# Kernel optimization log

Measured on AMD Instinct MI355X. Metric: run time of the kernel, lower is better.

The kernel has to match this reference:

```python
import jax, jax.numpy as jnp
import numpy as np

N_DIRS = 32  # number of projection directions


def gram_schmidt(x):
    # x: [B, n, D]; sequential Gram-Schmidt; normalized basis vectors are
    # detached (stop_gradient) as in the torch original.
    B, n, D = x.shape
    xs = jnp.swapaxes(x, 0, 1)  # [n, B, D]
    basis0 = jnp.zeros((n, B, D), dtype=x.dtype)

    def step(carry, w):
        basis, i = carry

        def proj(j, wv):
            b = basis[j]  # rows >= i are zero and contribute nothing
            return wv - b * jnp.sum(wv * b, axis=-1, keepdims=True)

        w_o = jax.lax.fori_loop(0, n, proj, w)
        w_sg = jax.lax.stop_gradient(w_o)
        w_hat = w_sg / jnp.linalg.norm(w_sg, axis=-1, keepdims=True)
        basis = jax.lax.dynamic_update_slice(basis, w_hat[None], (i, 0, 0))
        return (basis, i + 1), w_o

    (_, _), x_orth = jax.lax.scan(step, (basis0, jnp.int32(0)), xs)
    return jnp.swapaxes(x_orth, 0, 1)  # [B, n, D]


def setup_inputs() -> dict:
    key = jax.random.key(0)
    k = jax.random.split(key, 6)
    B = 2048
    IN_LP = 32 * 26       # 832 = linear_projection_x_dim * 26
    IMG = 28 * 28         # 784
    IN_NET = 2 * IMG      # 1568
    OUT_NET = N_DIRS * IMG  # 25088

    x_distorted = jax.random.normal(k[0], (B, IN_LP), dtype=jnp.float32)
    x_restored = jax.random.uniform(k[1], (B, 1, 28, 28), dtype=jnp.float32)

    s1 = 1.0 / np.sqrt(IN_LP)
    W_lp = jax.random.uniform(k[2], (IMG, IN_LP), jnp.float32, -s1, s1)
    b_lp = jax.random.uniform(k[3], (IMG,), jnp.float32, -s1, s1)

    s2 = 1.0 / np.sqrt(IN_NET)
    W_net = jax.random.uniform(k[4], (OUT_NET, IN_NET), jnp.float32, -s2, s2)
    b_net = jax.random.uniform(k[5], (OUT_NET,), jnp.float32, -s2, s2)

    return {"x_distorted": x_distorted, "x_restored": x_restored,
            "W_lp": W_lp, "b_lp": b_lp, "W_net": W_net, "b_net": b_net}


def reference(x_distorted, x_restored, W_lp, b_lp, W_net, b_net):
    B = x_distorted.shape[0]
    xd = x_distorted.reshape(B, -1) @ W_lp.T + b_lp      # [B, 784]
    xd = xd.reshape(B, 1, 28, 28)
    x = jnp.concatenate([xd, x_restored], axis=1)        # [B, 2, 28, 28]
    x = (x - 0.5) / 0.2
    w_mat = (x.reshape(B, -1) @ W_net.T + b_net) * 0.2   # [B, n_dirs*784]
    w_mat = w_mat.reshape(B, N_DIRS, -1)                 # [B, n_dirs, 784]
    return gram_schmidt(w_mat)
```

## Files before the change

### kernel.cpp

```cpp
#include <hip/hip_runtime.h>
#include <hip/hip_bf16.h>
#include <stdint.h>


typedef short s16x8 __attribute__((ext_vector_type(8)));
typedef float f32x4 __attribute__((ext_vector_type(4)));

#define GL_LDS16(gptr, lptr)                                                   \
    __builtin_amdgcn_global_load_lds(                                          \
        (const __attribute__((address_space(1))) void*)(gptr),                 \
        (__attribute__((address_space(3))) void*)(lptr), 16, 0, 0)

#define KP 1600

__global__ __launch_bounds__(512, 1) void gemm_mfma_256(
    const __hip_bfloat16* __restrict__ A, const __hip_bfloat16* __restrict__ B,
    const float* __restrict__ bias, float* __restrict__ C,
    int M, int N, int K)
{
    __shared__ __align__(16) short lds[2][30720];

    const int t = threadIdx.x;
    const int l = t & 63;
    const int wv = t >> 6;
    const int wm = wv >> 1;
    const int wn = wv & 1;

    const int f  = blockIdx.x;
    const int xb = f >> 3;
    const int yb = f & 7;
    const int m0 = yb * 256;
    const int n0 = xb * 224;

    const short* As = (const short*)A;
    const short* Bs = (const short*)B;

    const bool isA = wv < 4;
    const int colE = (((l & 7) ^ (l >> 3)) << 3);
    const size_t srcRow = isA ? (size_t)(m0 + wv * 64 + (l >> 3))
                              : (size_t)(n0 + (wv - 4) * 56 + (l >> 3));
    const size_t src0 = srcRow * KP + colE;
    const short* gsrc = isA ? As : Bs;
    const int dstBase = isA ? wv * 4096 : 16384 + (wv - 4) * 3584;

    const int sk0 = ((l >> 4) << 3) ^ ((l & 7) << 3);
    const int sk1 = sk0 ^ 32;
    const int aoff = (wm * 64 + (l & 15)) * 64;
    const int boff = 16384 + (wn * 112 + (l & 15)) * 64;

    f32x4 acc[4][7] = {};

#define STAGE_TILE(buf, T)                                                     \
    do {                                                                       \
        short* d_ = &lds[buf][dstBase];                                        \
        const short* s_ = gsrc + src0 + (size_t)(T) * 64;                      \
        GL_LDS16(s_ + (size_t)0 * 8 * KP, d_ + 0 * 512);                       \
        GL_LDS16(s_ + (size_t)1 * 8 * KP, d_ + 1 * 512);                       \
        GL_LDS16(s_ + (size_t)2 * 8 * KP, d_ + 2 * 512);                       \
        GL_LDS16(s_ + (size_t)3 * 8 * KP, d_ + 3 * 512);                       \
        GL_LDS16(s_ + (size_t)4 * 8 * KP, d_ + 4 * 512);                       \
        GL_LDS16(s_ + (size_t)5 * 8 * KP, d_ + 5 * 512);                       \
        GL_LDS16(s_ + (size_t)6 * 8 * KP, d_ + 6 * 512);                       \
        if (isA) GL_LDS16(s_ + (size_t)7 * 8 * KP, d_ + 7 * 512);              \
    } while (0)

    const int NT = K >> 6;
    STAGE_TILE(0, 0);
    __syncthreads();

    for (int kt = 0; kt < NT; ++kt) {
        const int cur = kt & 1;
        const short* bufc = &lds[cur][0];

        if (kt + 1 < NT) STAGE_TILE(cur ^ 1, kt + 1);

        s16x8 bfr[7][2];
        #pragma unroll
        for (int ni = 0; ni < 7; ++ni) {
            bfr[ni][0] = *(const s16x8*)&bufc[boff + ni * 1024 + sk0];
            bfr[ni][1] = *(const s16x8*)&bufc[boff + ni * 1024 + sk1];
        }

        #pragma unroll
        for (int mi = 0; mi < 4; ++mi) {
            s16x8 a0 = *(const s16x8*)&bufc[aoff + mi * 1024 + sk0];
            s16x8 a1 = *(const s16x8*)&bufc[aoff + mi * 1024 + sk1];
            __builtin_amdgcn_s_setprio(1);
            #pragma unroll
            for (int ni = 0; ni < 7; ++ni) {
                acc[mi][ni] = __builtin_amdgcn_mfma_f32_16x16x32_bf16(
                    a0, bfr[ni][0], acc[mi][ni], 0, 0, 0);
                acc[mi][ni] = __builtin_amdgcn_mfma_f32_16x16x32_bf16(
                    a1, bfr[ni][1], acc[mi][ni], 0, 0, 0);
            }
            __builtin_amdgcn_s_setprio(0);
        }

        __syncthreads();
    }
#undef STAGE_TILE

    const int row0 = m0 + wm * 64 + ((l >> 4) << 2);
    const int col0 = n0 + wn * 112 + (l & 15);
    #pragma unroll
    for (int ni = 0; ni < 7; ++ni) {
        const int n = col0 + ni * 16;
        const float bn = bias[n];
        #pragma unroll
        for (int mi = 0; mi < 4; ++mi) {
            const int r0 = row0 + mi * 16;
            #pragma unroll
            for (int r = 0; r < 4; ++r)
                C[(size_t)(r0 + r) * N + n] = (acc[mi][ni][r] + bn) * 0.2f;
        }
    }
}

__global__ __launch_bounds__(256) void wnet_to_bf16(
    const float* __restrict__ in, __hip_bfloat16* __restrict__ out)
{
    const size_t r = blockIdx.x;
    const int t = threadIdx.x;
    const float* src = in + r * 1568;
    __hip_bfloat16* dst = out + r * KP;

    for (int i = t; i < 392; i += 256) {
        float4 v = *(const float4*)(src + (i << 2));
        __hip_bfloat16 o[4] = {
            __float2bfloat16(v.x), __float2bfloat16(v.y),
            __float2bfloat16(v.z), __float2bfloat16(v.w)};
        *(ushort4*)&dst[i << 2] = *(const ushort4*)o;
    }
    if (t < 8)
        *(ushort4*)&dst[1568 + (t << 2)] = make_ushort4(0, 0, 0, 0);
}

#define TILE_M 64
#define TILE_N 64
#define TILE_K 16
#define LDS_STRIDE 72

__global__ __launch_bounds__(256) void gemm_nt_lp(
    const float* __restrict__ A, const float* __restrict__ B,
    const float* __restrict__ bias, __hip_bfloat16* __restrict__ C,
    int M, int N, int K, int ldc)
{
    __shared__ float As[TILE_K][LDS_STRIDE];
    __shared__ float Bsh[TILE_K][LDS_STRIDE];

    const int t  = threadIdx.x;
    const int tx = t & 15;
    const int ty = t >> 4;
    const int m0 = blockIdx.y * TILE_M;
    const int n0 = blockIdx.x * TILE_N;
    const int lrow = t >> 2;
    const int lk   = (t & 3) << 2;

    float acc[4][4] = {};

    for (int kt = 0; kt < K; kt += TILE_K) {
        float4 av = *(const float4*)(A + (size_t)(m0 + lrow) * K + kt + lk);
        float4 bv = make_float4(0.f, 0.f, 0.f, 0.f);
        if (n0 + lrow < N)
            bv = *(const float4*)(B + (size_t)(n0 + lrow) * K + kt + lk);

        __syncthreads();
        As[lk + 0][lrow] = av.x; As[lk + 1][lrow] = av.y;
        As[lk + 2][lrow] = av.z; As[lk + 3][lrow] = av.w;
        Bsh[lk + 0][lrow] = bv.x; Bsh[lk + 1][lrow] = bv.y;
        Bsh[lk + 2][lrow] = bv.z; Bsh[lk + 3][lrow] = bv.w;
        __syncthreads();

        #pragma unroll
        for (int k = 0; k < TILE_K; ++k) {
            float4 a = *(const float4*)&As[k][ty << 2];
            float4 b = *(const float4*)&Bsh[k][tx << 2];
            acc[0][0] += a.x * b.x; acc[0][1] += a.x * b.y;
            acc[0][2] += a.x * b.z; acc[0][3] += a.x * b.w;
            acc[1][0] += a.y * b.x; acc[1][1] += a.y * b.y;
            acc[1][2] += a.y * b.z; acc[1][3] += a.y * b.w;
            acc[2][0] += a.z * b.x; acc[2][1] += a.z * b.y;
            acc[2][2] += a.z * b.z; acc[2][3] += a.z * b.w;
            acc[3][0] += a.w * b.x; acc[3][1] += a.w * b.y;
            acc[3][2] += a.w * b.z; acc[3][3] += a.w * b.w;
        }
    }

    #pragma unroll
    for (int j = 0; j < 4; ++j) {
        int n = n0 + (tx << 2) + j;
        if (n < N) {
            float bn = bias[n];
            #pragma unroll
            for (int i = 0; i < 4; ++i) {
                float v = (acc[i][j] + bn - 0.5f) / 0.2f;
                C[(size_t)(m0 + (ty << 2) + i) * ldc + n] = __float2bfloat16(v);
            }
        }
    }
}

__global__ __launch_bounds__(256) void build_restored(
    const float* __restrict__ xr, __hip_bfloat16* __restrict__ x)
{
    const int b = blockIdx.x;
    const int t = threadIdx.x;
    if (t < 196) {
        float4 v = *(const float4*)(xr + (size_t)b * 784 + (t << 2));
        __hip_bfloat16 o[4] = {
            __float2bfloat16((v.x - 0.5f) / 0.2f),
            __float2bfloat16((v.y - 0.5f) / 0.2f),
            __float2bfloat16((v.z - 0.5f) / 0.2f),
            __float2bfloat16((v.w - 0.5f) / 0.2f)};
        *(ushort4*)&x[(size_t)b * KP + 784 + (t << 2)] = *(const ushort4*)o;
    } else if (t < 204) {
        *(ushort4*)&x[(size_t)b * KP + 1568 + ((t - 196) << 2)] =
            make_ushort4(0, 0, 0, 0);
    }
}

#define GS_N 32
#define GS_D 784

__global__ __launch_bounds__(256, 4) void gram_solve(
    const float* __restrict__ out, float* __restrict__ Mws)
{
    __shared__ __align__(16) short Wc[GS_N * 64];
    __shared__ float Gs[GS_N][GS_N + 1];
    __shared__ float Ms[GS_N][GS_N + 1];
    __shared__ float Ld[GS_N];

    const int t = threadIdx.x;
    const int l = t & 63;
    const int w = t >> 6;
    const float* row0 = out + (size_t)blockIdx.x * (GS_N * GS_D);

    const int wr = w >> 1, wc2 = w & 1;
    const int ra = wr * 16 + (l & 15);
    const int rb = wc2 * 16 + (l & 15);
    const int kg = l >> 4;

    f32x4 acc = {};

    for (int k0 = 0; k0 < 832; k0 += 64) {
        #pragma unroll
        for (int hh = 0; hh < 2; ++hh) {
            const int h   = t + hh * 256;
            const int r   = h >> 4;
            const int hg  = h & 15;
            const int col = k0 + (hg << 2);
            ushort4 u = make_ushort4(0, 0, 0, 0);
            if (col < GS_D) {
                float4 v = *(const float4*)(row0 + r * GS_D + col);
                __hip_bfloat16 hb[4] = {
                    __float2bfloat16(v.x), __float2bfloat16(v.y),
                    __float2bfloat16(v.z), __float2bfloat16(v.w)};
                u = *(const ushort4*)hb;
            }
            const int gp = (hg >> 1) ^ (r & 7);
            *(ushort4*)&Wc[(r << 6) + (gp << 3) + ((hg & 1) << 2)] = u;
        }
        __syncthreads();

        #pragma unroll
        for (int s = 0; s < 2; ++s) {
            const int ga = ((s << 2) + kg) ^ (ra & 7);
            const int gb = ((s << 2) + kg) ^ (rb & 7);
            s16x8 af = *(const s16x8*)&Wc[(ra << 6) + (ga << 3)];
            s16x8 bf = *(const s16x8*)&Wc[(rb << 6) + (gb << 3)];
            acc = __builtin_amdgcn_mfma_f32_16x16x32_bf16(af, bf, acc, 0, 0, 0);
        }
        __syncthreads();
    }

    {
        const int di = wr * 16 + (l >> 4) * 4;
        const int dj = wc2 * 16 + (l & 15);
        #pragma unroll
        for (int r = 0; r < 4; ++r) Gs[di + r][dj] = acc[r];
    }
    for (int z = t; z < GS_N * (GS_N + 1); z += 256) ((float*)Ms)[z] = 0.f;
    __syncthreads();

    for (int k = 0; k < GS_N; ++k) {
        const float sk = sqrtf(Gs[k][k]);
        if (t == k) Ld[k] = sk;
        if (t > k && t < GS_N) Gs[t][k] /= sk;
        __syncthreads();
        if (t > k && t < GS_N) {
            const float lik = Gs[t][k];
            for (int j = k + 1; j <= t; ++j)
                Gs[t][j] -= lik * Gs[j][k];
        }
        __syncthreads();
    }

    if (t < GS_N) {
        const int j = t;
        Ms[j][j] = 1.0f / Ld[j];
        for (int i = j + 1; i < GS_N; ++i) {
            float a = 0.f;
            for (int k = j; k < i; ++k)
                a += Gs[i][k] * Ms[k][j];
            Ms[i][j] = -a / Ld[i];
        }
        for (int i = j + 1; i < GS_N; ++i)
            Ms[i][j] *= Ld[i];
    }
    __syncthreads();

    {
        const int i = t >> 3, j0 = (t & 7) << 2;
        float4 mv = make_float4(Ms[i][j0], Ms[i][j0 + 1],
                                Ms[i][j0 + 2], Ms[i][j0 + 3]);
        *(float4*)(Mws + (size_t)blockIdx.x * 1024 + (t << 2)) = mv;
    }
}

__global__ __launch_bounds__(256, 8) void gs_apply(
    float* __restrict__ out, const float* __restrict__ Mws)
{
    __shared__ float4 Wf[GS_N][28];
    __shared__ float  Ml[GS_N][36];

    const int t = threadIdx.x;
    const int b = blockIdx.y;
    const int k0 = blockIdx.x * 112;
    float* row0 = out + (size_t)b * (GS_N * GS_D);

    {
        float4 mv = *(const float4*)(Mws + (size_t)b * 1024 + (t << 2));
        const int i = t >> 3, j0 = (t & 7) << 2;
        *(float4*)&Ml[i][j0] = mv;
    }
    #pragma unroll
    for (int hh = 0; hh < 4; ++hh) {
        const int h = t + hh * 256;
        const int r = h >> 5, c = h & 31;
        if (c < 28)
            Wf[r][c] = *(const float4*)(row0 + r * GS_D + k0 + (c << 2));
    }
    __syncthreads();

    const int g  = t >> 5;
    const int c4 = t & 31;
    if (c4 < 28) {
        const int rA = g, rB = 31 - g, rC = 15 - g, rD = 16 + g;
        float4 vA = Wf[rA][c4];
        float4 vB = Wf[rB][c4];
        float4 vC = Wf[rC][c4];
        float4 vD = Wf[rD][c4];
        for (int j = 0; j < rB; ++j) {
            const float4 wj = Wf[j][c4];
            const float mA = (j < rA) ? Ml[rA][j] : 0.f;
            const float mB = Ml[rB][j];
            vA.x += mA * wj.x; vA.y += mA * wj.y;
            vA.z += mA * wj.z; vA.w += mA * wj.w;
            vB.x += mB * wj.x; vB.y += mB * wj.y;
            vB.z += mB * wj.z; vB.w += mB * wj.w;
        }
        for (int j = 0; j < rD; ++j) {
            const float4 wj = Wf[j][c4];
            const float mC = (j < rC) ? Ml[rC][j] : 0.f;
            const float mD = Ml[rD][j];
            vC.x += mC * wj.x; vC.y += mC * wj.y;
            vC.z += mC * wj.z; vC.w += mC * wj.w;
            vD.x += mD * wj.x; vD.y += mD * wj.y;
            vD.z += mD * wj.z; vD.w += mD * wj.w;
        }
        *(float4*)(row0 + rA * GS_D + k0 + (c4 << 2)) = vA;
        *(float4*)(row0 + rB * GS_D + k0 + (c4 << 2)) = vB;
        *(float4*)(row0 + rC * GS_D + k0 + (c4 << 2)) = vC;
        *(float4*)(row0 + rD * GS_D + k0 + (c4 << 2)) = vD;
    }
}

extern "C" void kernel_launch(void* const* d_in, const int* in_sizes, int n_in,
                              void* d_out, int out_size, void* d_ws, size_t ws_size,
                              hipStream_t stream)
{
    const float* xd   = (const float*)d_in[0];
    const float* xr   = (const float*)d_in[1];
    const float* Wlp  = (const float*)d_in[2];
    const float* blp  = (const float*)d_in[3];
    const float* Wnet = (const float*)d_in[4];
    const float* bnet = (const float*)d_in[5];
    float* out = (float*)d_out;

    const int B = 2048, IN_LP = 832, IMG = 784, OUT = 32 * 784;

    __hip_bfloat16* Wnet_bf = (__hip_bfloat16*)d_ws;
    __hip_bfloat16* x_bf =
        (__hip_bfloat16*)((char*)d_ws + (size_t)OUT * KP * 2);
    float* Mws = (float*)d_ws;

    wnet_to_bf16<<<OUT, 256, 0, stream>>>(Wnet, Wnet_bf);

    gemm_nt_lp<<<dim3((IMG + TILE_N - 1) / TILE_N, B / TILE_M), 256, 0, stream>>>(
        xd, Wlp, blp, x_bf, B, IMG, IN_LP, KP);

    build_restored<<<B, 256, 0, stream>>>(xr, x_bf);

    gemm_mfma_256<<<dim3(896), 512, 0, stream>>>(
        x_bf, Wnet_bf, bnet, out, B, OUT, KP);

    gram_solve<<<B, 256, 0, stream>>>(out, Mws);

    gs_apply<<<dim3(7, B), 256, 0, stream>>>(out, Mws);
}
```

Before: 448.1 us.

## Merge prep kernels into one launch and load Gram inputs directly into registers

Combines the W_net bf16 conversion, the small linear-projection GEMM and the restored-image packing into a single launch, with block-range dispatch picking the job for each block. This removes two kernel launches and the gaps between them. Separately, gram_solve now loads fp32 rows straight from global memory into MFMA operands, converting in registers, and drops the LDS staging and its barriers. The direct loads are less coalesced and the same rows are reread by several waves, which may raise memory traffic.

```diff
diff --git a/kernel.cpp b/kernel.cpp
--- a/kernel.cpp
+++ b/kernel.cpp
@@ -116,116 +116,126 @@
     }
 }
 
-__global__ __launch_bounds__(256) void wnet_to_bf16(
-    const float* __restrict__ in, __hip_bfloat16* __restrict__ out)
-{
-    const size_t r = blockIdx.x;
-    const int t = threadIdx.x;
-    const float* src = in + r * 1568;
-    __hip_bfloat16* dst = out + r * KP;
-
-    for (int i = t; i < 392; i += 256) {
-        float4 v = *(const float4*)(src + (i << 2));
-        __hip_bfloat16 o[4] = {
-            __float2bfloat16(v.x), __float2bfloat16(v.y),
-            __float2bfloat16(v.z), __float2bfloat16(v.w)};
-        *(ushort4*)&dst[i << 2] = *(const ushort4*)o;
-    }
-    if (t < 8)
-        *(ushort4*)&dst[1568 + (t << 2)] = make_ushort4(0, 0, 0, 0);
-}
-
 #define TILE_M 64
 #define TILE_N 64
 #define TILE_K 16
 #define LDS_STRIDE 72
-
-__global__ __launch_bounds__(256) void gemm_nt_lp(
-    const float* __restrict__ A, const float* __restrict__ B,
-    const float* __restrict__ bias, __hip_bfloat16* __restrict__ C,
-    int M, int N, int K, int ldc)
+#define NB_K1 416
+#define NB_K2 2048
+#define NB_K0 25088
+
+__global__ __launch_bounds__(256) void prep012(
+    const float* __restrict__ xd, const float* __restrict__ xr,
+    const float* __restrict__ Wlp, const float* __restrict__ blp,
+    const float* __restrict__ Wnet,
+    __hip_bfloat16* __restrict__ Wnet_bf, __hip_bfloat16* __restrict__ x_bf)
 {
-    __shared__ float As[TILE_K][LDS_STRIDE];
-    __shared__ float Bsh[TILE_K][LDS_STRIDE];
-
-    const int t  = threadIdx.x;
-    const int tx = t & 15;
-    const int ty = t >> 4;
-    const int m0 = blockIdx.y * TILE_M;
-    const int n0 = blockIdx.x * TILE_N;
-    const int lrow = t >> 2;
-    const int lk   = (t & 3) << 2;
-
-    float acc[4][4] = {};
-
-    for (int kt = 0; kt < K; kt += TILE_K) {
-        float4 av = *(const float4*)(A + (size_t)(m0 + lrow) * K + kt + lk);
-        float4 bv = make_float4(0.f, 0.f, 0.f, 0.f);
-        if (n0 + lrow < N)
-            bv = *(const float4*)(B + (size_t)(n0 + lrow) * K + kt + lk);
-
-        __syncthreads();
-        As[lk + 0][lrow] = av.x; As[lk + 1][lrow] = av.y;
-        As[lk + 2][lrow] = av.z; As[lk + 3][lrow] = av.w;
-        Bsh[lk + 0][lrow] = bv.x; Bsh[lk + 1][lrow] = bv.y;
-        Bsh[lk + 2][lrow] = bv.z; Bsh[lk + 3][lrow] = bv.w;
-        __syncthreads();
+    const int bid = blockIdx.x;
+    const int t = threadIdx.x;
+
+    if (bid < NB_K1) {
+        __shared__ float As[TILE_K][LDS_STRIDE];
+        __shared__ float Bsh[TILE_K][LDS_STRIDE];
+
+        const int bx = bid % 13, by = bid / 13;
+        const int tx = t & 15;
+        const int ty = t >> 4;
+        const int m0 = by * TILE_M;
+        const int n0 = bx * TILE_N;
+        const int lrow = t >> 2;
+        const int lk   = (t & 3) << 2;
+        const int Kd = 832, Nd = 784;
+
+        float acc[4][4] = {};
+
+        for (int kt = 0; kt < Kd; kt += TILE_K) {
+            float4 av = *(const float4*)(xd + (size_t)(m0 + lrow) * Kd + kt + lk);
+            float4 bv = make_float4(0.f, 0.f, 0.f, 0.f);
+            if (n0 + lrow < Nd)
+                bv = *(const float4*)(Wlp + (size_t)(n0 + lrow) * Kd + kt + lk);
+
+            __syncthreads();
+            As[lk + 0][lrow] = av.x; As[lk + 1][lrow] = av.y;
+            As[lk + 2][lrow] = av.z; As[lk + 3][lrow] = av.w;
+            Bsh[lk + 0][lrow] = bv.x; Bsh[lk + 1][lrow] = bv.y;
+            Bsh[lk + 2][lrow] = bv.z; Bsh[lk + 3][lrow] = bv.w;
+            __syncthreads();
+
+            #pragma unroll
+            for (int k = 0; k < TILE_K; ++k) {
+                float4 a = *(const float4*)&As[k][ty << 2];
+                float4 b = *(const float4*)&Bsh[k][tx << 2];
+                acc[0][0] += a.x * b.x; acc[0][1] += a.x * b.y;
+                acc[0][2] += a.x * b.z; acc[0][3] += a.x * b.w;
+                acc[1][0] += a.y * b.x; acc[1][1] += a.y * b.y;
+                acc[1][2] += a.y * b.z; acc[1][3] += a.y * b.w;
+                acc[2][0] += a.z * b.x; acc[2][1] += a.z * b.y;
+                acc[2][2] += a.z * b.z; acc[2][3] += a.z * b.w;
+                acc[3][0] += a.w * b.x; acc[3][1] += a.w * b.y;
+                acc[3][2] += a.w * b.z; acc[3][3] += a.w * b.w;
+            }
+        }
 
         #pragma unroll
-        for (int k = 0; k < TILE_K; ++k) {
-            float4 a = *(const float4*)&As[k][ty << 2];
-            float4 b = *(const float4*)&Bsh[k][tx << 2];
-            acc[0][0] += a.x * b.x; acc[0][1] += a.x * b.y;
-            acc[0][2] += a.x * b.z; acc[0][3] += a.x * b.w;
-            acc[1][0] += a.y * b.x; acc[1][1] += a.y * b.y;
-            acc[1][2] += a.y * b.z; acc[1][3] += a.y * b.w;
-            acc[2][0] += a.z * b.x; acc[2][1] += a.z * b.y;
-            acc[2][2] += a.z * b.z; acc[2][3] += a.z * b.w;
-            acc[3][0] += a.w * b.x; acc[3][1] += a.w * b.y;
-            acc[3][2] += a.w * b.z; acc[3][3] += a.w * b.w;
-        }
-    }
-
-    #pragma unroll
-    for (int j = 0; j < 4; ++j) {
-        int n = n0 + (tx << 2) + j;
-        if (n < N) {
-            float bn = bias[n];
-            #pragma unroll
-            for (int i = 0; i < 4; ++i) {
-                float v = (acc[i][j] + bn - 0.5f) / 0.2f;
-                C[(size_t)(m0 + (ty << 2) + i) * ldc + n] = __float2bfloat16(v);
+        for (int j = 0; j < 4; ++j) {
+            int n = n0 + (tx << 2) + j;
+            if (n < Nd) {
+                float bn = blp[n];
+                #pragma unroll
+                for (int i = 0; i < 4; ++i) {
+                    float v = (acc[i][j] + bn - 0.5f) / 0.2f;
+                    x_bf[(size_t)(m0 + (ty << 2) + i) * KP + n] =
+                        __float2bfloat16(v);
+                }
             }
         }
-    }
-}
-
-__global__ __launch_bounds__(256) void build_restored(
-    const float* __restrict__ xr, __hip_bfloat16* __restrict__ x)
-{
-    const int b = blockIdx.x;
-    const int t = threadIdx.x;
-    if (t < 196) {
-        float4 v = *(const float4*)(xr + (size_t)b * 784 + (t << 2));
-        __hip_bfloat16 o[4] = {
-            __float2bfloat16((v.x - 0.5f) / 0.2f),
-            __float2bfloat16((v.y - 0.5f) / 0.2f),
-            __float2bfloat16((v.z - 0.5f) / 0.2f),
-            __float2bfloat16((v.w - 0.5f) / 0.2f)};
-        *(ushort4*)&x[(size_t)b * KP + 784 + (t << 2)] = *(const ushort4*)o;
-    } else if (t < 204) {
-        *(ushort4*)&x[(size_t)b * KP + 1568 + ((t - 196) << 2)] =
-            make_ushort4(0, 0, 0, 0);
+    } else if (bid < NB_K1 + NB_K2) {
+        const int b = bid - NB_K1;
+        if (t < 196) {
+            float4 v = *(const float4*)(xr + (size_t)b * 784 + (t << 2));
+            __hip_bfloat16 o[4] = {
+                __float2bfloat16((v.x - 0.5f) / 0.2f),
+                __float2bfloat16((v.y - 0.5f) / 0.2f),
+                __float2bfloat16((v.z - 0.5f) / 0.2f),
+                __float2bfloat16((v.w - 0.5f) / 0.2f)};
+            *(ushort4*)&x_bf[(size_t)b * KP + 784 + (t << 2)] =
+                *(const ushort4*)o;
+        } else if (t < 204) {
+            *(ushort4*)&x_bf[(size_t)b * KP + 1568 + ((t - 196) << 2)] =
+                make_ushort4(0, 0, 0, 0);
+        }
+    } else {
+        const size_t r = bid - (NB_K1 + NB_K2);
+        const float* src = Wnet + r * 1568;
+        __hip_bfloat16* dst = Wnet_bf + r * KP;
+
+        for (int i = t; i < 392; i += 256) {
+            float4 v = *(const float4*)(src + (i << 2));
+            __hip_bfloat16 o[4] = {
+                __float2bfloat16(v.x), __float2bfloat16(v.y),
+                __float2bfloat16(v.z), __float2bfloat16(v.w)};
+            *(ushort4*)&dst[i << 2] = *(const ushort4*)o;
+        }
+        if (t < 8)
+            *(ushort4*)&dst[1568 + (t << 2)] = make_ushort4(0, 0, 0, 0);
     }
 }
 
 #define GS_N 32
 #define GS_D 784
+
+__device__ __forceinline__ s16x8 cvt8(float4 a, float4 b) {
+    __hip_bfloat16 h[8] = {
+        __float2bfloat16(a.x), __float2bfloat16(a.y),
+        __float2bfloat16(a.z), __float2bfloat16(a.w),
+        __float2bfloat16(b.x), __float2bfloat16(b.y),
+        __float2bfloat16(b.z), __float2bfloat16(b.w)};
+    return *(const s16x8*)h;
+}
 
 __global__ __launch_bounds__(256, 4) void gram_solve(
     const float* __restrict__ out, float* __restrict__ Mws)
 {
-    __shared__ __align__(16) short Wc[GS_N * 64];
     __shared__ float Gs[GS_N][GS_N + 1];
     __shared__ float Ms[GS_N][GS_N + 1];
     __shared__ float Ld[GS_N];
@@ -240,37 +250,29 @@
     const int rb = wc2 * 16 + (l & 15);
     const int kg = l >> 4;
 
+    const float* pa = row0 + (size_t)ra * GS_D + kg * 8;
+    const float* pb = row0 + (size_t)rb * GS_D + kg * 8;
+
     f32x4 acc = {};
-
-    for (int k0 = 0; k0 < 832; k0 += 64) {
-        #pragma unroll
-        for (int hh = 0; hh < 2; ++hh) {
-            const int h   = t + hh * 256;
-            const int r   = h >> 4;
-            const int hg  = h & 15;
-            const int col = k0 + (hg << 2);
-            ushort4 u = make_ushort4(0, 0, 0, 0);
-            if (col < GS_D) {
-                float4 v = *(const float4*)(row0 + r * GS_D + col);
-                __hip_bfloat16 hb[4] = {
-                    __float2bfloat16(v.x), __float2bfloat16(v.y),
-                    __float2bfloat16(v.z), __float2bfloat16(v.w)};
-                u = *(const ushort4*)hb;
-            }
-            const int gp = (hg >> 1) ^ (r & 7);
-            *(ushort4*)&Wc[(r << 6) + (gp << 3) + ((hg & 1) << 2)] = u;
-        }
-        __syncthreads();
-
-        #pragma unroll
-        for (int s = 0; s < 2; ++s) {
-            const int ga = ((s << 2) + kg) ^ (ra & 7);
-            const int gb = ((s << 2) + kg) ^ (rb & 7);
-            s16x8 af = *(const s16x8*)&Wc[(ra << 6) + (ga << 3)];
-            s16x8 bf = *(const s16x8*)&Wc[(rb << 6) + (gb << 3)];
-            acc = __builtin_amdgcn_mfma_f32_16x16x32_bf16(af, bf, acc, 0, 0, 0);
-        }
-        __syncthreads();
+    #pragma unroll 2
+    for (int s = 0; s < 24; ++s) {
+        float4 a0 = *(const float4*)(pa + s * 32);
+        float4 a1 = *(const float4*)(pa + s * 32 + 4);
+        float4 b0 = *(const float4*)(pb + s * 32);
+        float4 b1 = *(const float4*)(pb + s * 32 + 4);
+        acc = __builtin_amdgcn_mfma_f32_16x16x32_bf16(
+            cvt8(a0, a1), cvt8(b0, b1), acc, 0, 0, 0);
+    }
+    {
+        s16x8 af = {}, bf = {};
+        if (kg < 2) {
+            float4 a0 = *(const float4*)(pa + 768);
+            float4 a1 = *(const float4*)(pa + 768 + 4);
+            float4 b0 = *(const float4*)(pb + 768);
+            float4 b1 = *(const float4*)(pb + 768 + 4);
+            af = cvt8(a0, a1); bf = cvt8(b0, b1);
+        }
+        acc = __builtin_amdgcn_mfma_f32_16x16x32_bf16(af, bf, acc, 0, 0, 0);
     }
 
     {
@@ -387,19 +389,15 @@
     const float* bnet = (const float*)d_in[5];
     float* out = (float*)d_out;
 
-    const int B = 2048, IN_LP = 832, IMG = 784, OUT = 32 * 784;
+    const int B = 2048, OUT = 32 * 784;
 
     __hip_bfloat16* Wnet_bf = (__hip_bfloat16*)d_ws;
     __hip_bfloat16* x_bf =
         (__hip_bfloat16*)((char*)d_ws + (size_t)OUT * KP * 2);
     float* Mws = (float*)d_ws;
 
-    wnet_to_bf16<<<OUT, 256, 0, stream>>>(Wnet, Wnet_bf);
-
-    gemm_nt_lp<<<dim3((IMG + TILE_N - 1) / TILE_N, B / TILE_M), 256, 0, stream>>>(
-        xd, Wlp, blp, x_bf, B, IMG, IN_LP, KP);
-
-    build_restored<<<B, 256, 0, stream>>>(xr, x_bf);
+    prep012<<<NB_K1 + NB_K2 + NB_K0, 256, 0, stream>>>(
+        xd, xr, Wlp, blp, Wnet, Wnet_bf, x_bf);
 
     gemm_mfma_256<<<dim3(896), 512, 0, stream>>>(
         x_bf, Wnet_bf, bnet, out, B, OUT, KP);
```

Measured after the change: 440.9 us (median of 2 runs). About the same (-1.6%).
